# Optimization experiments

Measured on AMD Instinct MI355X. Metric: run time of the kernel, lower is better.

Reference implementation:

```python
import jax, jax.numpy as jnp
import numpy as np

C = 128      # hidden_channels
H = 4        # heads
DH = C // H
G = 4096     # num genes (segments)
R = 4096     # num reactions
E = 65536    # total (reaction, gene) pairs
LMAX = 64    # padded segment length
NB = 4       # blocks: 2 encoder SABs + 1 PMA + 1 decoder SAB
EPS = 1e-5


def _ln(x, g, b):
    m = jnp.mean(x, axis=-1, keepdims=True)
    v = jnp.mean((x - m) ** 2, axis=-1, keepdims=True)
    return (x - m) * jax.lax.rsqrt(v + EPS) * g + b


def setup_inputs() -> dict:
    key = jax.random.key(0)
    ks = jax.random.split(key, 12)
    sc = 1.0 / np.sqrt(C)
    zb = jnp.zeros((NB, C), jnp.float32)
    ob = jnp.ones((NB, C), jnp.float32)
    # every gene gets >= 1 reaction (matches realistic GEM mapping; avoids empty segments)
    gene_idx = jnp.sort(jnp.concatenate([
        jnp.arange(G, dtype=jnp.int32),
        jax.random.randint(ks[8], (E - G,), 0, G, jnp.int32)]))
    return {
        'reaction_features': jax.random.normal(ks[0], (R, C), jnp.float32),
        'Wq': jax.random.normal(ks[1], (NB, C, C), jnp.float32) * sc,
        'Wk': jax.random.normal(ks[2], (NB, C, C), jnp.float32) * sc,
        'Wv': jax.random.normal(ks[3], (NB, C, C), jnp.float32) * sc,
        'Wo': jax.random.normal(ks[4], (NB, C, C), jnp.float32) * sc,
        'bq': zb, 'bk': zb, 'bv': zb, 'bo': zb,
        'Wlin': jax.random.normal(ks[5], (NB, C, C), jnp.float32) * sc,
        'blin': zb,
        'g1': ob, 'b1': zb, 'g2': ob, 'b2': zb,
        'seed': jax.random.normal(ks[6], (1, 1, C), jnp.float32) * sc,
        'rxn_idx': jax.random.randint(ks[7], (E,), 0, R, jnp.int32),
        'gene_idx': gene_idx,
        'num_genes': G,
        'Lmax': LMAX,
    }


def _forward(reaction_features, Wq, Wk, Wv, Wo, bq, bk, bv, bo, Wlin, blin,
             g1, b1, g2, b2, seed, rxn_idx, gene_idx, num_genes, Lmax):
    E_ = gene_idx.shape[0]
    feats = reaction_features[rxn_idx]                      # [E, C] gather
    counts = jax.ops.segment_sum(jnp.ones((E_,), jnp.int32), gene_idx,
                                 num_segments=num_genes)
    starts = jnp.cumsum(counts) - counts                    # first flat index of each segment
    pos = jnp.arange(E_, dtype=jnp.int32) - starts[gene_idx]
    # to_dense_batch: [G, Lmax, C] + mask
    x = jnp.zeros((num_genes, Lmax, C), feats.dtype).at[gene_idx, pos].set(feats, mode='drop')
    mask = jnp.zeros((num_genes, Lmax), bool).at[gene_idx, pos].set(True, mode='drop')

    def mab(q_in, kv_in, q_mask, kv_mask, i):
        B, Lq, _ = q_in.shape
        Lk = kv_in.shape[1]
        q = (q_in @ Wq[i] + bq[i]).reshape(B, Lq, H, DH)
        k = (kv_in @ Wk[i] + bk[i]).reshape(B, Lk, H, DH)
        v = (kv_in @ Wv[i] + bv[i]).reshape(B, Lk, H, DH)
        scores = jnp.einsum('bqhd,bkhd->bhqk', q, k) / np.sqrt(DH)
        if kv_mask is not None:
            scores = jnp.where(kv_mask[:, None, None, :], scores, -1e30)
        a = jax.nn.softmax(scores, axis=-1)
        attn = jnp.einsum('bhqk,bkhd->bqhd', a, v).reshape(B, Lq, C) @ Wo[i] + bo[i]
        if q_mask is not None:
            attn = jnp.where(q_mask[:, :, None], attn, 0.0)
        out = _ln(attn + q_in, g1[i], b1[i])
        out = out + jax.nn.relu(out @ Wlin[i] + blin[i])
        return _ln(out, g2[i], b2[i])

    h = mab(x, x, mask, mask, 0)          # encoder SAB 1
    h = mab(h, h, mask, mask, 1)          # encoder SAB 2
    s = jnp.broadcast_to(seed, (num_genes, seed.shape[1], C))
    h = mab(s, h, None, mask, 2)          # PMA (1 seed point)
    h = mab(h, h, None, None, 3)          # decoder SAB
    h = jnp.nan_to_num(h)
    return h.reshape(num_genes, -1)       # [G, C] (concat over 1 seed)


def reference(reaction_features, Wq, Wk, Wv, Wo, bq, bk, bv, bo, Wlin, blin,
              g1, b1, g2, b2, seed, rxn_idx, gene_idx, num_genes, Lmax):
    return _forward(reaction_features, Wq, Wk, Wv, Wo, bq, bk, bv, bo, Wlin,
                    blin, g1, b1, g2, b2, seed, rxn_idx, gene_idx, num_genes, Lmax)
```

## Files before the change

### kernel.cpp

```cpp
#include <hip/hip_runtime.h>
#include <hip/hip_bf16.h>
#include <math.h>

#define C 128
#define H 4
#define LMAX 64
#define EPS 1e-5f
#define ISQ 0.17677669529663687f

using short8  = __attribute__((ext_vector_type(8))) short;
using short4v = __attribute__((ext_vector_type(4))) short;
using f32x4   = __attribute__((ext_vector_type(4))) float;

__device__ __forceinline__ float wsum(float v){
  #pragma unroll
  for (int o = 32; o > 0; o >>= 1) v += __shfl_xor(v, o, 64);
  return v;
}
__device__ __forceinline__ float wmax(float v){
  #pragma unroll
  for (int o = 32; o > 0; o >>= 1) v = fmaxf(v, __shfl_xor(v, o, 64));
  return v;
}
__device__ __forceinline__ short f2bs(float f){
  __hip_bfloat16 b = __float2bfloat16(f);
  union { __hip_bfloat16 b; short u; } cv; cv.b = b; return cv.u;
}
__device__ __forceinline__ float b2f(short u){
  return __uint_as_float(((unsigned)(unsigned short)u) << 16);
}

__global__ void prep_wfrag(const float* __restrict__ Wq, const float* __restrict__ Wk,
                           const float* __restrict__ Wv, const float* __restrict__ Wo,
                           const float* __restrict__ Wlin, short* __restrict__ wf){
  int bid = blockIdx.x, l = threadIdx.x;
  int tile = bid & 31, mb = bid >> 5;
  int mat = mb >> 2, blk = mb & 3;
  const float* W = (mat==0?Wq : mat==1?Wk : mat==2?Wv : mat==3?Wo : Wlin) + blk*C*C;
  int nt = tile >> 2, kt = tile & 3;
  int col = nt*16 + (l & 15);
  int k0  = kt*32 + ((l >> 4) << 3);
  short8 v;
  #pragma unroll
  for (int j = 0; j < 8; j++) v[j] = f2bs(W[(k0 + j)*C + col]);
  *(short8*)(wf + ((size_t)mb*32 + tile)*512 + (size_t)l*8) = v;
}

__global__ void prep_qrow(const float* __restrict__ seed, const float* __restrict__ Wq,
                          const float* __restrict__ bq, float* __restrict__ qrow){
  int t = threadIdx.x;
  const float* wq2 = Wq + 2*C*C;
  float acc = bq[2*C + t];
  #pragma unroll 4
  for (int k = 0; k < C; k++) acc = fmaf(seed[k], wq2[k*C + t], acc);
  qrow[t] = acc;
}

__global__ void seg_kernel(const int* __restrict__ gidx, int E, int G,
                           int* __restrict__ starts, int* __restrict__ counts,
                           int* __restrict__ cnt, int* __restrict__ gcr){
  int g = blockIdx.x * blockDim.x + threadIdx.x;
  if (g >= G) return;
  int lo = 0, hi = E;
  while (lo < hi){ int m = (lo + hi) >> 1; if (gidx[m] < g) lo = m + 1; else hi = m; }
  int s = lo; hi = E;
  while (lo < hi){ int m = (lo + hi) >> 1; if (gidx[m] < g + 1) lo = m + 1; else hi = m; }
  starts[g] = s;
  int c_ = lo - s; counts[g] = c_;
  int L = c_ > LMAX ? LMAX : c_; if (L < 1) L = 1;
  int cl = (L - 1) >> 4;
  int r = atomicAdd(&cnt[cl], 1);
  gcr[g] = (cl << 28) | r;
}

__global__ void fill_kernel(int G, const int* __restrict__ cnt, const int* __restrict__ gcr,
                            int* __restrict__ binfo, int* __restrict__ nbins){
  int g = blockIdx.x * blockDim.x + threadIdx.x;
  if (g >= G) return;
  int nb1 = (cnt[0] + 3) >> 2, nb2 = (cnt[1] + 1) >> 1, nb3 = cnt[2];
  if (g == 0) *nbins = nb1 + nb2 + nb3 + cnt[3];
  int v = gcr[g]; int cl = v >> 28; int r = v & 0x0FFFFFFF;
  int bin, slot;
  if      (cl == 0){ bin = r >> 2;             slot = r & 3; }
  else if (cl == 1){ bin = nb1 + (r >> 1);     slot = (r & 1) * 2; }
  else if (cl == 2){ bin = nb1 + nb2 + r;      slot = 0; }
  else             { bin = nb1 + nb2 + nb3 + r; slot = 0; }
  binfo[bin*4 + slot] = g;
}

__device__ __forceinline__ f32x4 mfma4(short8 a0, short8 a1, short8 a2, short8 a3,
                                       const short* __restrict__ wf, int nt, int l){
  f32x4 acc = {0.f, 0.f, 0.f, 0.f};
  acc = __builtin_amdgcn_mfma_f32_16x16x32_bf16(a0, *(const short8*)(wf + ((nt*4+0)*64 + l)*8), acc, 0,0,0);
  acc = __builtin_amdgcn_mfma_f32_16x16x32_bf16(a1, *(const short8*)(wf + ((nt*4+1)*64 + l)*8), acc, 0,0,0);
  acc = __builtin_amdgcn_mfma_f32_16x16x32_bf16(a2, *(const short8*)(wf + ((nt*4+2)*64 + l)*8), acc, 0,0,0);
  acc = __builtin_amdgcn_mfma_f32_16x16x32_bf16(a3, *(const short8*)(wf + ((nt*4+3)*64 + l)*8), acc, 0,0,0);
  return acc;
}

__device__ __forceinline__ void ln_rows(const short (*src)[136], short (*dst)[136],
                                        const float* __restrict__ gg,
                                        const float* __restrict__ bb, int t){
  int row = t >> 2, q4 = t & 3;
  float v[32];
  float sm = 0.f;
  #pragma unroll
  for (int kk = 0; kk < 32; ++kk){
    float x = b2f(src[row][q4*32 + kk]);
    v[kk] = x; sm += x;
  }
  sm += __shfl_xor(sm, 1);
  sm += __shfl_xor(sm, 2);
  float mean = sm * (1.f/128.f);
  float s2 = 0.f;
  #pragma unroll
  for (int kk = 0; kk < 32; ++kk){ float d = v[kk] - mean; s2 += d*d; }
  s2 += __shfl_xor(s2, 1);
  s2 += __shfl_xor(s2, 2);
  float rs = rsqrtf(s2*(1.f/128.f) + EPS);
  #pragma unroll
  for (int kk = 0; kk < 32; ++kk){
    int col = q4*32 + kk;
    dst[row][col] = f2bs((v[kk] - mean)*rs*gg[col] + bb[col]);
  }
}

__global__ __launch_bounds__(256, 2) void gene_bin_kernel(
  const float* __restrict__ RF, const short* __restrict__ wfrag,
  const float* __restrict__ qrow,
  const float* __restrict__ bq, const float* __restrict__ bk,
  const float* __restrict__ bv, const float* __restrict__ bo,
  const float* __restrict__ blin,
  const float* __restrict__ g1, const float* __restrict__ b1,
  const float* __restrict__ g2, const float* __restrict__ b2,
  const int* __restrict__ rxn_idx, const int* __restrict__ starts,
  const int* __restrict__ counts, const int* __restrict__ binfo,
  const int* __restrict__ meta, float* __restrict__ pooled)
{
  if ((int)blockIdx.x >= meta[0]) return;
  __shared__ short xb[64][136];
  __shared__ short qb[64][136];
  __shared__ short kb[64][136];
  __shared__ short vt[128][72];
  __shared__ __align__(16) short sc[64][72];
  __shared__ float qrl[C];
  __shared__ int mg[4], mL[4], ms0[4], mbase[4];

  const int bin = blockIdx.x;
  const int t = threadIdx.x, w = t >> 6, l = t & 63;
  const int hi = l >> 4, c = l & 15;

  if (t == 0){
    int s = 0;
    while (s < 4){
      int g = binfo[bin*4 + s];
      if (g >= 0){
        int Lg = counts[g]; if (Lg > LMAX) Lg = LMAX;
        int ntg = (Lg + 15) >> 4;
        for (int u = 0; u < ntg; ++u){ mg[s+u] = g; mL[s+u] = Lg; ms0[s+u] = starts[g]; mbase[s+u] = s; }
        s += ntg;
      } else { mg[s] = -1; mL[s] = 0; ms0[s] = 0; mbase[s] = s; s++; }
    }
  }
  if (t < C) qrl[t] = qrow[t];
  __syncthreads();

  for (int idx = t; idx < 64*16; idx += 256){
    int row = idx >> 4, ch = idx & 15;
    int s = row >> 4;
    int g = mg[s];
    int ro = row - mbase[s]*16;
    short8 u = {0,0,0,0,0,0,0,0};
    if (g >= 0 && ro < mL[s]){
      int rr = rxn_idx[ms0[s] + ro];
      const float* src = RF + (size_t)rr*C + ch*8;
      float4 v0 = *(const float4*)(src);
      float4 v1 = *(const float4*)(src + 4);
      u[0]=f2bs(v0.x); u[1]=f2bs(v0.y); u[2]=f2bs(v0.z); u[3]=f2bs(v0.w);
      u[4]=f2bs(v1.x); u[5]=f2bs(v1.y); u[6]=f2bs(v1.z); u[7]=f2bs(v1.w);
    }
    *(short8*)&xb[row][ch*8] = u;
  }
  {
    short8 z = {0,0,0,0,0,0,0,0};
    for (int idx = t; idx < 64*9; idx += 256){
      int row = idx / 9, ch = idx - row*9;
      *(short8*)&sc[row][ch*8] = z;
    }
  }
  __syncthreads();

  for (int blk = 0; blk < 2; ++blk){
    {
      short8 ax[4][4];
      #pragma unroll
      for (int mt = 0; mt < 4; ++mt)
        #pragma unroll
        for (int kk = 0; kk < 4; ++kk)
          ax[mt][kk] = *(const short8*)&xb[mt*16 + c][kk*32 + hi*8];
      #pragma unroll
      for (int i = 0; i < 6; ++i){
        int pr = w + 4*i;
        int mat = pr >> 3, nt = pr & 7;
        const short* wfm = wfrag + (size_t)(mat*4 + blk)*16384;
        const float* bias = (mat == 0 ? bq : mat == 1 ? bk : bv);
        int col = nt*16 + c;
        float bb = bias[blk*C + col];
        #pragma unroll
        for (int mt = 0; mt < 4; ++mt){
          f32x4 acc = mfma4(ax[mt][0], ax[mt][1], ax[mt][2], ax[mt][3], wfm, nt, l);
          if (mat == 2){
            short4v pk;
            #pragma unroll
            for (int r = 0; r < 4; r++) pk[r] = f2bs(acc[r] + bb);
            *(short4v*)&vt[col][mt*16 + hi*4] = pk;
          } else if (mat == 0){
            #pragma unroll
            for (int r = 0; r < 4; r++) qb[mt*16 + hi*4 + r][col] = f2bs(acc[r] + bb);
          } else {
            #pragma unroll
            for (int r = 0; r < 4; r++) kb[mt*16 + hi*4 + r][col] = f2bs(acc[r] + bb);
          }
        }
      }
    }
    __syncthreads();

    for (int h = 0; h < H; ++h){
      for (int idx = w; idx < 16; idx += 4){
        int mt = idx >> 2, kt = idx & 3;
        int gm = mg[mt];
        if (gm >= 0 && gm == mg[kt]){
          short8 a = *(const short8*)&qb[mt*16 + c][h*32 + hi*8];
          short8 b = *(const short8*)&kb[kt*16 + c][h*32 + hi*8];
          f32x4 acc = {0.f, 0.f, 0.f, 0.f};
          acc = __builtin_amdgcn_mfma_f32_16x16x32_bf16(a, b, acc, 0,0,0);
          #pragma unroll
          for (int r = 0; r < 4; r++) sc[mt*16 + hi*4 + r][kt*16 + c] = f2bs(acc[r] * ISQ);
        }
      }
      __syncthreads();
      {
        int row = t >> 2, q4 = t & 3;
        int s = row >> 4;
        if (mg[s] >= 0){
          int kbeg = mbase[s]*16;
          int kend = kbeg + mL[s];
          int send = kbeg + (((mL[s] + 15) >> 4) << 4);
          int b0 = q4*16;
          float e[16];
          float mx = -3.4e38f;
          #pragma unroll
          for (int kk = 0; kk < 16; ++kk){
            int col = b0 + kk;
            bool ok = (col >= kbeg) && (col < kend);
            float lg = ok ? b2f(sc[row][col]) : -3.4e38f;
            e[kk] = lg;
            mx = fmaxf(mx, lg);
          }
          mx = fmaxf(mx, __shfl_xor(mx, 1));
          mx = fmaxf(mx, __shfl_xor(mx, 2));
          float sm = 0.f;
          #pragma unroll
          for (int kk = 0; kk < 16; ++kk){
            int col = b0 + kk;
            bool ok = (col >= kbeg) && (col < kend);
            float ee = ok ? __expf(e[kk] - mx) : 0.f;
            e[kk] = ee; sm += ee;
          }
          sm += __shfl_xor(sm, 1);
          sm += __shfl_xor(sm, 2);
          float inv = 1.f / sm;
          #pragma unroll
          for (int kk = 0; kk < 16; ++kk){
            int col = b0 + kk;
            if (col >= kbeg && col < send)
              sc[row][col] = f2bs((col < kend) ? e[kk]*inv : 0.f);
          }
        }
      }
      __syncthreads();
      for (int idx = w; idx < 8; idx += 4){
        int mt = idx >> 1, dt = idx & 1;
        if (mg[mt] >= 0){
          f32x4 acc = {0.f, 0.f, 0.f, 0.f};
          #pragma unroll
          for (int ks = 0; ks < 2; ++ks){
            short8 a = *(const short8*)&sc[mt*16 + c][ks*32 + hi*8];
            short8 b = *(const short8*)&vt[h*32 + dt*16 + c][ks*32 + hi*8];
            acc = __builtin_amdgcn_mfma_f32_16x16x32_bf16(a, b, acc, 0,0,0);
          }
          int col = h*32 + dt*16 + c;
          #pragma unroll
          for (int r = 0; r < 4; r++) qb[mt*16 + hi*4 + r][col] = f2bs(acc[r]);
        }
      }
      __syncthreads();
    }

    {
      short8 aw[4];
      #pragma unroll
      for (int kk = 0; kk < 4; kk++) aw[kk] = *(const short8*)&qb[w*16 + c][kk*32 + hi*8];
      const short* wfo = wfrag + (size_t)(3*4 + blk)*16384;
      #pragma unroll 2
      for (int nt = 0; nt < 8; ++nt){
        int col = nt*16 + c;
        f32x4 acc = mfma4(aw[0], aw[1], aw[2], aw[3], wfo, nt, l);
        float bb = bo[blk*C + col];
        #pragma unroll
        for (int r = 0; r < 4; r++){
          int row = w*16 + hi*4 + r;
          xb[row][col] = f2bs(acc[r] + bb + b2f(xb[row][col]));
        }
      }
    }
    __syncthreads();
    ln_rows(xb, xb, g1 + blk*C, b1 + blk*C, t);
    __syncthreads();

    {
      short8 aw[4];
      #pragma unroll
      for (int kk = 0; kk < 4; kk++) aw[kk] = *(const short8*)&xb[w*16 + c][kk*32 + hi*8];
      const short* wfl = wfrag + (size_t)(4*4 + blk)*16384;
      #pragma unroll 2
      for (int nt = 0; nt < 8; ++nt){
        int col = nt*16 + c;
        f32x4 acc = mfma4(aw[0], aw[1], aw[2], aw[3], wfl, nt, l);
        float bb = blin[blk*C + col];
        #pragma unroll
        for (int r = 0; r < 4; r++){
          int row = w*16 + hi*4 + r;
          kb[row][col] = f2bs(b2f(xb[row][col]) + fmaxf(acc[r] + bb, 0.f));
        }
      }
    }
    __syncthreads();
    ln_rows(kb, xb, g2 + blk*C, b2 + blk*C, t);
    __syncthreads();
  }

  {
    short8 aw[4];
    #pragma unroll
    for (int kk = 0; kk < 4; kk++) aw[kk] = *(const short8*)&xb[w*16 + c][kk*32 + hi*8];
    const short* wfk2 = wfrag + (size_t)(1*4 + 2)*16384;
    const short* wfv2 = wfrag + (size_t)(2*4 + 2)*16384;
    #pragma unroll 2
    for (int nt = 0; nt < 8; ++nt){
      int col = nt*16 + c;
      f32x4 acc = mfma4(aw[0], aw[1], aw[2], aw[3], wfk2, nt, l);
      float bb = bk[2*C + col];
      #pragma unroll
      for (int r = 0; r < 4; r++) kb[w*16 + hi*4 + r][col] = f2bs(acc[r] + bb);
      acc = mfma4(aw[0], aw[1], aw[2], aw[3], wfv2, nt, l);
      bb = bv[2*C + col];
      short4v pk;
      #pragma unroll
      for (int r = 0; r < 4; r++) pk[r] = f2bs(acc[r] + bb);
      *(short4v*)&vt[col][w*16 + hi*4] = pk;
    }
  }
  __syncthreads();
  {
    int g = mg[w];
    if (g >= 0 && mbase[w] == w){
      int L = mL[w];
      int row = w*16 + l;
      float* ps = (float*)&sc[0][0];
      #pragma unroll
      for (int h = 0; h < 4; ++h){
        float a = -3.4e38f;
        if (l < L){
          float acc = 0.f;
          #pragma unroll 8
          for (int dd = 0; dd < 32; ++dd)
            acc = fmaf(b2f(kb[row][h*32 + dd]), qrl[h*32 + dd], acc);
          a = acc * ISQ;
        }
        float mx = wmax(a);
        float e = (l < L) ? __expf(a - mx) : 0.f;
        float s = wsum(e);
        ps[(w*4 + h)*64 + l] = e / s;
      }
      #pragma unroll
      for (int half = 0; half < 2; ++half){
        int d = l + half*64;
        int h = d >> 5;
        float acc = 0.f;
        for (int kk = 0; kk < L; ++kk)
          acc = fmaf(ps[(w*4 + h)*64 + kk], b2f(vt[d][w*16 + kk]), acc);
        pooled[(size_t)g*C + d] = acc;
      }
    }
  }
}

__global__ __launch_bounds__(256) void tail_kernel(
  const float* __restrict__ pooled,
  const float* __restrict__ Wv, const float* __restrict__ Wo,
  const float* __restrict__ Wlin,
  const float* __restrict__ bv, const float* __restrict__ bo,
  const float* __restrict__ blin,
  const float* __restrict__ g1, const float* __restrict__ b1,
  const float* __restrict__ g2, const float* __restrict__ b2,
  const float* __restrict__ seed, float* __restrict__ out)
{
  __shared__ float row0[C], row1[C], row2[C];
  const int g = blockIdx.x, t = threadIdx.x, w = t >> 6, l = t & 63;
  if (t < C) row1[t] = pooled[(size_t)g*C + t];
  __syncthreads();
  if (t < C){
    float acc = bo[2*C + t];
    const float* wo2 = Wo + 2*C*C;
    #pragma unroll 4
    for (int k = 0; k < C; k++) acc = fmaf(row1[k], wo2[k*C + t], acc);
    row0[t] = acc + seed[t];
  }
  __syncthreads();
  if (w == 0){
    float v0 = row0[l], v1 = row0[l + 64];
    float m = wsum(v0 + v1) * (1.f / C);
    float d0 = v0 - m, d1 = v1 - m;
    float va = wsum(d0*d0 + d1*d1) * (1.f / C);
    float rs = rsqrtf(va + EPS);
    row0[l]      = d0 * rs * g1[2*C + l]      + b1[2*C + l];
    row0[l + 64] = d1 * rs * g1[2*C + l + 64] + b1[2*C + l + 64];
  }
  __syncthreads();
  if (t < C){
    float acc = blin[2*C + t];
    const float* wl2 = Wlin + 2*C*C;
    #pragma unroll 4
    for (int k = 0; k < C; k++) acc = fmaf(row0[k], wl2[k*C + t], acc);
    row1[t] = row0[t] + fmaxf(acc, 0.f);
  }
  __syncthreads();
  if (w == 0){
    float v0 = row1[l], v1 = row1[l + 64];
    float m = wsum(v0 + v1) * (1.f / C);
    float d0 = v0 - m, d1 = v1 - m;
    float va = wsum(d0*d0 + d1*d1) * (1.f / C);
    float rs = rsqrtf(va + EPS);
    row0[l]      = d0 * rs * g2[2*C + l]      + b2[2*C + l];
    row0[l + 64] = d1 * rs * g2[2*C + l + 64] + b2[2*C + l + 64];
  }
  __syncthreads();
  {
    const float* wv3 = Wv + 3*C*C; const float* wo3 = Wo + 3*C*C; const float* wl3 = Wlin + 3*C*C;
    if (t < C){
      float acc = bv[3*C + t];
      #pragma unroll 4
      for (int k = 0; k < C; k++) acc = fmaf(row0[k], wv3[k*C + t], acc);
      row1[t] = acc;
    }
    __syncthreads();
    if (t < C){
      float acc = bo[3*C + t];
      #pragma unroll 4
      for (int k = 0; k < C; k++) acc = fmaf(row1[k], wo3[k*C + t], acc);
      row2[t] = acc + row0[t];
    }
    __syncthreads();
    if (w == 0){
      float v0 = row2[l], v1 = row2[l + 64];
      float m = wsum(v0 + v1) * (1.f / C);
      float d0 = v0 - m, d1 = v1 - m;
      float va = wsum(d0*d0 + d1*d1) * (1.f / C);
      float rs = rsqrtf(va + EPS);
      row2[l]      = d0 * rs * g1[3*C + l]      + b1[3*C + l];
      row2[l + 64] = d1 * rs * g1[3*C + l + 64] + b1[3*C + l + 64];
    }
    __syncthreads();
    if (t < C){
      float acc = blin[3*C + t];
      #pragma unroll 4
      for (int k = 0; k < C; k++) acc = fmaf(row2[k], wl3[k*C + t], acc);
      row1[t] = row2[t] + fmaxf(acc, 0.f);
    }
    __syncthreads();
    if (w == 0){
      float v0 = row1[l], v1 = row1[l + 64];
      float m = wsum(v0 + v1) * (1.f / C);
      float d0 = v0 - m, d1 = v1 - m;
      float va = wsum(d0*d0 + d1*d1) * (1.f / C);
      float rs = rsqrtf(va + EPS);
      float r0 = d0 * rs * g2[3*C + l]      + b2[3*C + l];
      float r1 = d1 * rs * g2[3*C + l + 64] + b2[3*C + l + 64];
      if (isnan(r0)) r0 = 0.f; else if (isinf(r0)) r0 = r0 > 0 ? 3.402823466e38f : -3.402823466e38f;
      if (isnan(r1)) r1 = 0.f; else if (isinf(r1)) r1 = r1 > 0 ? 3.402823466e38f : -3.402823466e38f;
      out[(size_t)g*C + l]      = r0;
      out[(size_t)g*C + l + 64] = r1;
    }
  }
}

extern "C" void kernel_launch(void* const* d_in, const int* in_sizes, int n_in,
                              void* d_out, int out_size, void* d_ws, size_t ws_size,
                              hipStream_t stream){
  const float* RF   = (const float*)d_in[0];
  const float* Wq   = (const float*)d_in[1];
  const float* Wk   = (const float*)d_in[2];
  const float* Wv   = (const float*)d_in[3];
  const float* Wo   = (const float*)d_in[4];
  const float* bq   = (const float*)d_in[5];
  const float* bk   = (const float*)d_in[6];
  const float* bv   = (const float*)d_in[7];
  const float* bo   = (const float*)d_in[8];
  const float* Wlin = (const float*)d_in[9];
  const float* blin = (const float*)d_in[10];
  const float* g1   = (const float*)d_in[11];
  const float* b1   = (const float*)d_in[12];
  const float* g2   = (const float*)d_in[13];
  const float* b2   = (const float*)d_in[14];
  const float* seed = (const float*)d_in[15];
  const int* rxn    = (const int*)d_in[16];
  const int* gidx   = (const int*)d_in[17];

  int E = in_sizes[16];
  int G = out_size / C;

  char* base = (char*)d_ws;
  short* wfrag = (short*)base;
  float* qrow  = (float*)(base + 655360);
  int*   meta  = (int*)(base + 655872);
  int*   starts= (int*)(base + 655936);
  int*   counts= (int*)(base + 655936 + (size_t)4*G);
  int*   gcr   = (int*)(base + 655936 + (size_t)8*G);
  int*   binfo = (int*)(base + 655936 + (size_t)12*G);
  float* pooled= (float*)(base + 655936 + (size_t)28*G);

  hipMemsetAsync(meta, 0, 64, stream);
  hipMemsetAsync(binfo, 0xFF, (size_t)16*G, stream);
  prep_wfrag<<<640, 64, 0, stream>>>(Wq, Wk, Wv, Wo, Wlin, wfrag);
  prep_qrow<<<1, 128, 0, stream>>>(seed, Wq, bq, qrow);
  seg_kernel<<<(G + 255)/256, 256, 0, stream>>>(gidx, E, G, starts, counts, meta + 1, gcr);
  fill_kernel<<<(G + 255)/256, 256, 0, stream>>>(G, meta + 1, gcr, binfo, meta);
  gene_bin_kernel<<<G, 256, 0, stream>>>(RF, wfrag, qrow, bq, bk, bv, bo, blin,
      g1, b1, g2, b2, rxn, starts, counts, binfo, meta, pooled);
  tail_kernel<<<G, 256, 0, stream>>>(pooled, Wv, Wo, Wlin, bv, bo, blin,
      g1, b1, g2, b2, seed, (float*)d_out);
}
```

Measured before the change: 310.1 us.

## Restructure gene-bin kernel per-wave with in-register softmax/LN and batch tail kernel

The gene-bin kernel now gives each wave its own 16-row tile. Q/K/V projection, attention scores, softmax, layernorm and the residual all stay in registers, which removes the score scratch buffer and most block-wide barriers. Shared memory shrinks (qb, sc and qrl are dropped, rows are padded to 138) and occupancy is raised to 3 blocks per SM. PV MFMAs are skipped for key tiles outside the segment. The tail kernel now handles 16 genes per block, so weight reads are amortised across rows, at the cost of higher register pressure and more intricate per-wave LDS reuse.

```diff
diff --git a/kernel.cpp b/kernel.cpp
--- a/kernel.cpp
+++ b/kernel.cpp
@@ -3,14 +3,14 @@
 #include <math.h>
 
 #define C 128
-#define H 4
 #define LMAX 64
 #define EPS 1e-5f
 #define ISQ 0.17677669529663687f
 
 using short8  = __attribute__((ext_vector_type(8))) short;
-using short4v = __attribute__((ext_vector_type(4))) short;
 using f32x4   = __attribute__((ext_vector_type(4))) float;
+
+#define WSYNC() do { asm volatile("s_waitcnt lgkmcnt(0)" ::: "memory"); __builtin_amdgcn_sched_barrier(0); } while(0)
 
 __device__ __forceinline__ float wsum(float v){
   #pragma unroll
@@ -28,6 +28,9 @@
 }
 __device__ __forceinline__ float b2f(short u){
   return __uint_as_float(((unsigned)(unsigned short)u) << 16);
+}
+__device__ __forceinline__ unsigned pack2(float a, float b){
+  return (unsigned)(unsigned short)f2bs(a) | ((unsigned)(unsigned short)f2bs(b) << 16);
 }
 
 __global__ void prep_wfrag(const float* __restrict__ Wq, const float* __restrict__ Wk,
@@ -98,34 +101,25 @@
   return acc;
 }
 
-__device__ __forceinline__ void ln_rows(const short (*src)[136], short (*dst)[136],
-                                        const float* __restrict__ gg,
-                                        const float* __restrict__ bb, int t){
-  int row = t >> 2, q4 = t & 3;
-  float v[32];
-  float sm = 0.f;
-  #pragma unroll
-  for (int kk = 0; kk < 32; ++kk){
-    float x = b2f(src[row][q4*32 + kk]);
-    v[kk] = x; sm += x;
-  }
-  sm += __shfl_xor(sm, 1);
-  sm += __shfl_xor(sm, 2);
-  float mean = sm * (1.f/128.f);
-  float s2 = 0.f;
-  #pragma unroll
-  for (int kk = 0; kk < 32; ++kk){ float d = v[kk] - mean; s2 += d*d; }
-  s2 += __shfl_xor(s2, 1);
-  s2 += __shfl_xor(s2, 2);
-  float rs = rsqrtf(s2*(1.f/128.f) + EPS);
-  #pragma unroll
-  for (int kk = 0; kk < 32; ++kk){
-    int col = q4*32 + kk;
-    dst[row][col] = f2bs((v[kk] - mean)*rs*gg[col] + bb[col]);
-  }
-}
-
-__global__ __launch_bounds__(256, 2) void gene_bin_kernel(
+__device__ __forceinline__ void ln_inreg(float (&v)[8][4], const float (&gv)[8], const float (&bv)[8]){
+  #pragma unroll
+  for (int r = 0; r < 4; ++r){
+    float s = 0.f;
+    #pragma unroll
+    for (int nt = 0; nt < 8; ++nt) s += v[nt][r];
+    s += __shfl_xor(s,1); s += __shfl_xor(s,2); s += __shfl_xor(s,4); s += __shfl_xor(s,8);
+    float mean = s * (1.f/128.f);
+    float q = 0.f;
+    #pragma unroll
+    for (int nt = 0; nt < 8; ++nt){ float d = v[nt][r] - mean; q += d*d; }
+    q += __shfl_xor(q,1); q += __shfl_xor(q,2); q += __shfl_xor(q,4); q += __shfl_xor(q,8);
+    float rs = rsqrtf(q*(1.f/128.f) + EPS);
+    #pragma unroll
+    for (int nt = 0; nt < 8; ++nt) v[nt][r] = (v[nt][r] - mean)*rs*gv[nt] + bv[nt];
+  }
+}
+
+__global__ __launch_bounds__(256, 3) void gene_bin_kernel(
   const float* __restrict__ RF, const short* __restrict__ wfrag,
   const float* __restrict__ qrow,
   const float* __restrict__ bq, const float* __restrict__ bk,
@@ -137,18 +131,16 @@
   const int* __restrict__ counts, const int* __restrict__ binfo,
   const int* __restrict__ meta, float* __restrict__ pooled)
 {
+  __shared__ short xb[64][138];
+  __shared__ short kb[64][138];
+  __shared__ short vt[128][74];
+  __shared__ int mg[4], mL[4], ms0[4], mbase[4];
+
   if ((int)blockIdx.x >= meta[0]) return;
-  __shared__ short xb[64][136];
-  __shared__ short qb[64][136];
-  __shared__ short kb[64][136];
-  __shared__ short vt[128][72];
-  __shared__ __align__(16) short sc[64][72];
-  __shared__ float qrl[C];
-  __shared__ int mg[4], mL[4], ms0[4], mbase[4];
-
   const int bin = blockIdx.x;
   const int t = threadIdx.x, w = t >> 6, l = t & 63;
   const int hi = l >> 4, c = l & 15;
+  const int r0 = w * 16;
 
   if (t == 0){
     int s = 0;
@@ -162,7 +154,6 @@
       } else { mg[s] = -1; mL[s] = 0; ms0[s] = 0; mbase[s] = s; s++; }
     }
   }
-  if (t < C) qrl[t] = qrow[t];
   __syncthreads();
 
   for (int idx = t; idx < 64*16; idx += 256){
@@ -181,220 +172,271 @@
     }
     *(short8*)&xb[row][ch*8] = u;
   }
-  {
-    short8 z = {0,0,0,0,0,0,0,0};
-    for (int idx = t; idx < 64*9; idx += 256){
-      int row = idx / 9, ch = idx - row*9;
-      *(short8*)&sc[row][ch*8] = z;
-    }
-  }
-  __syncthreads();
-
+  __syncthreads();
+
+  const int myg  = mg[w];
+  const int kbeg = mbase[w]*16;
+  const int kend = kbeg + mL[w];
+
+  float resid[8][4];
+  #pragma unroll
+  for (int nt = 0; nt < 8; ++nt)
+    #pragma unroll
+    for (int r = 0; r < 4; ++r)
+      resid[nt][r] = b2f(xb[r0 + hi*4 + r][nt*16 + c]);
+  WSYNC();
+
+  #pragma unroll 1
   for (int blk = 0; blk < 2; ++blk){
+    const short* wfq = wfrag + (size_t)(0*4 + blk)*16384;
+    const short* wfk = wfrag + (size_t)(1*4 + blk)*16384;
+    const short* wfv = wfrag + (size_t)(2*4 + blk)*16384;
+    const short* wfo = wfrag + (size_t)(3*4 + blk)*16384;
+    const short* wfl = wfrag + (size_t)(4*4 + blk)*16384;
+
     {
-      short8 ax[4][4];
-      #pragma unroll
-      for (int mt = 0; mt < 4; ++mt)
+      short8 ax[4];
+      #pragma unroll
+      for (int kk = 0; kk < 4; ++kk) ax[kk] = *(const short8*)&xb[r0 + c][kk*32 + hi*8];
+      WSYNC();
+      #pragma unroll
+      for (int nt = 0; nt < 8; ++nt){
+        int col = nt*16 + c;
+        f32x4 aq = mfma4(ax[0],ax[1],ax[2],ax[3], wfq, nt, l);
+        f32x4 ak = mfma4(ax[0],ax[1],ax[2],ax[3], wfk, nt, l);
+        f32x4 av = mfma4(ax[0],ax[1],ax[2],ax[3], wfv, nt, l);
+        float bqv = bq[blk*C + col], bkv = bk[blk*C + col], bvv = bv[blk*C + col];
         #pragma unroll
-        for (int kk = 0; kk < 4; ++kk)
-          ax[mt][kk] = *(const short8*)&xb[mt*16 + c][kk*32 + hi*8];
-      #pragma unroll
-      for (int i = 0; i < 6; ++i){
-        int pr = w + 4*i;
-        int mat = pr >> 3, nt = pr & 7;
-        const short* wfm = wfrag + (size_t)(mat*4 + blk)*16384;
-        const float* bias = (mat == 0 ? bq : mat == 1 ? bk : bv);
-        int col = nt*16 + c;
-        float bb = bias[blk*C + col];
+        for (int r = 0; r < 4; ++r){
+          kb[r0 + hi*4 + r][col] = f2bs(ak[r] + bkv);
+          vt[col][r0 + hi*4 + r] = f2bs(av[r] + bvv);
+          xb[r0 + hi*4 + r][col] = f2bs(aq[r] + bqv);
+        }
+      }
+    }
+    __syncthreads();
+
+    unsigned pp[4][8];
+    #pragma unroll
+    for (int h = 0; h < 4; ++h){
+      short8 qa = *(const short8*)&xb[r0 + c][h*32 + hi*8];
+      f32x4 lg[4];
+      #pragma unroll
+      for (int kt = 0; kt < 4; ++kt){
+        f32x4 z = {0.f,0.f,0.f,0.f};
+        if (myg >= 0 && mg[kt] == myg)
+          z = __builtin_amdgcn_mfma_f32_16x16x32_bf16(qa,
+                *(const short8*)&kb[kt*16 + c][h*32 + hi*8], z, 0,0,0);
+        lg[kt] = z;
+      }
+      float P[4][4];
+      #pragma unroll
+      for (int r = 0; r < 4; ++r){
+        float mx = -3.4e38f;
         #pragma unroll
-        for (int mt = 0; mt < 4; ++mt){
-          f32x4 acc = mfma4(ax[mt][0], ax[mt][1], ax[mt][2], ax[mt][3], wfm, nt, l);
-          if (mat == 2){
-            short4v pk;
-            #pragma unroll
-            for (int r = 0; r < 4; r++) pk[r] = f2bs(acc[r] + bb);
-            *(short4v*)&vt[col][mt*16 + hi*4] = pk;
-          } else if (mat == 0){
-            #pragma unroll
-            for (int r = 0; r < 4; r++) qb[mt*16 + hi*4 + r][col] = f2bs(acc[r] + bb);
-          } else {
-            #pragma unroll
-            for (int r = 0; r < 4; r++) kb[mt*16 + hi*4 + r][col] = f2bs(acc[r] + bb);
+        for (int kt = 0; kt < 4; ++kt){
+          int col = kt*16 + c;
+          bool ok = (col >= kbeg) && (col < kend);
+          float v = ok ? lg[kt][r]*ISQ : -3.4e38f;
+          P[kt][r] = v;
+          mx = fmaxf(mx, v);
+        }
+        mx = fmaxf(mx, __shfl_xor(mx,1)); mx = fmaxf(mx, __shfl_xor(mx,2));
+        mx = fmaxf(mx, __shfl_xor(mx,4)); mx = fmaxf(mx, __shfl_xor(mx,8));
+        float sm = 0.f;
+        #pragma unroll
+        for (int kt = 0; kt < 4; ++kt){
+          int col = kt*16 + c;
+          bool ok = (col >= kbeg) && (col < kend);
+          float e = ok ? __expf(P[kt][r] - mx) : 0.f;
+          P[kt][r] = e; sm += e;
+        }
+        sm += __shfl_xor(sm,1); sm += __shfl_xor(sm,2);
+        sm += __shfl_xor(sm,4); sm += __shfl_xor(sm,8);
+        float inv = (sm > 0.f) ? 1.f/sm : 0.f;
+        #pragma unroll
+        for (int kt = 0; kt < 4; ++kt) P[kt][r] *= inv;
+      }
+      #pragma unroll
+      for (int kt = 0; kt < 4; ++kt){
+        pp[h][kt*2+0] = pack2(P[kt][0], P[kt][1]);
+        pp[h][kt*2+1] = pack2(P[kt][2], P[kt][3]);
+      }
+    }
+    __syncthreads();
+
+    f32x4 O[8];
+    {
+      f32x4 zz = {0.f,0.f,0.f,0.f};
+      #pragma unroll
+      for (int nt = 0; nt < 8; ++nt) O[nt] = zz;
+    }
+    #pragma unroll
+    for (int pr = 0; pr < 2; ++pr){
+      #pragma unroll
+      for (int hh = 0; hh < 2; ++hh){
+        int h = pr*2 + hh;
+        #pragma unroll
+        for (int kt = 0; kt < 4; ++kt)
+          #pragma unroll
+          for (int r = 0; r < 4; ++r){
+            unsigned u = pp[h][kt*2 + (r>>1)];
+            xb[r0 + hi*4 + r][hh*64 + kt*16 + c] = (short)((r&1) ? (u >> 16) : (u & 0xFFFF));
           }
-        }
-      }
-    }
-    __syncthreads();
-
-    for (int h = 0; h < H; ++h){
-      for (int idx = w; idx < 16; idx += 4){
-        int mt = idx >> 2, kt = idx & 3;
-        int gm = mg[mt];
-        if (gm >= 0 && gm == mg[kt]){
-          short8 a = *(const short8*)&qb[mt*16 + c][h*32 + hi*8];
-          short8 b = *(const short8*)&kb[kt*16 + c][h*32 + hi*8];
-          f32x4 acc = {0.f, 0.f, 0.f, 0.f};
-          acc = __builtin_amdgcn_mfma_f32_16x16x32_bf16(a, b, acc, 0,0,0);
-          #pragma unroll
-          for (int r = 0; r < 4; r++) sc[mt*16 + hi*4 + r][kt*16 + c] = f2bs(acc[r] * ISQ);
-        }
-      }
-      __syncthreads();
-      {
-        int row = t >> 2, q4 = t & 3;
-        int s = row >> 4;
-        if (mg[s] >= 0){
-          int kbeg = mbase[s]*16;
-          int kend = kbeg + mL[s];
-          int send = kbeg + (((mL[s] + 15) >> 4) << 4);
-          int b0 = q4*16;
-          float e[16];
-          float mx = -3.4e38f;
-          #pragma unroll
-          for (int kk = 0; kk < 16; ++kk){
-            int col = b0 + kk;
-            bool ok = (col >= kbeg) && (col < kend);
-            float lg = ok ? b2f(sc[row][col]) : -3.4e38f;
-            e[kk] = lg;
-            mx = fmaxf(mx, lg);
-          }
-          mx = fmaxf(mx, __shfl_xor(mx, 1));
-          mx = fmaxf(mx, __shfl_xor(mx, 2));
-          float sm = 0.f;
-          #pragma unroll
-          for (int kk = 0; kk < 16; ++kk){
-            int col = b0 + kk;
-            bool ok = (col >= kbeg) && (col < kend);
-            float ee = ok ? __expf(e[kk] - mx) : 0.f;
-            e[kk] = ee; sm += ee;
-          }
-          sm += __shfl_xor(sm, 1);
-          sm += __shfl_xor(sm, 2);
-          float inv = 1.f / sm;
-          #pragma unroll
-          for (int kk = 0; kk < 16; ++kk){
-            int col = b0 + kk;
-            if (col >= kbeg && col < send)
-              sc[row][col] = f2bs((col < kend) ? e[kk]*inv : 0.f);
-          }
-        }
-      }
-      __syncthreads();
-      for (int idx = w; idx < 8; idx += 4){
-        int mt = idx >> 1, dt = idx & 1;
-        if (mg[mt] >= 0){
-          f32x4 acc = {0.f, 0.f, 0.f, 0.f};
+      }
+      WSYNC();
+      #pragma unroll
+      for (int hh = 0; hh < 2; ++hh){
+        int h = pr*2 + hh;
+        #pragma unroll
+        for (int dt = 0; dt < 2; ++dt){
+          f32x4 acc = O[h*2 + dt];
           #pragma unroll
           for (int ks = 0; ks < 2; ++ks){
-            short8 a = *(const short8*)&sc[mt*16 + c][ks*32 + hi*8];
-            short8 b = *(const short8*)&vt[h*32 + dt*16 + c][ks*32 + hi*8];
-            acc = __builtin_amdgcn_mfma_f32_16x16x32_bf16(a, b, acc, 0,0,0);
+            if (kend > ks*32 && kbeg < ks*32 + 32){
+              short8 a = *(const short8*)&xb[r0 + c][hh*64 + ks*32 + hi*8];
+              short8 b = *(const short8*)&vt[h*32 + dt*16 + c][ks*32 + hi*8];
+              acc = __builtin_amdgcn_mfma_f32_16x16x32_bf16(a, b, acc, 0,0,0);
+            }
           }
-          int col = h*32 + dt*16 + c;
-          #pragma unroll
-          for (int r = 0; r < 4; r++) qb[mt*16 + hi*4 + r][col] = f2bs(acc[r]);
+          O[h*2 + dt] = acc;
         }
       }
-      __syncthreads();
-    }
-
-    {
-      short8 aw[4];
-      #pragma unroll
-      for (int kk = 0; kk < 4; kk++) aw[kk] = *(const short8*)&qb[w*16 + c][kk*32 + hi*8];
-      const short* wfo = wfrag + (size_t)(3*4 + blk)*16384;
-      #pragma unroll 2
-      for (int nt = 0; nt < 8; ++nt){
-        int col = nt*16 + c;
-        f32x4 acc = mfma4(aw[0], aw[1], aw[2], aw[3], wfo, nt, l);
-        float bb = bo[blk*C + col];
-        #pragma unroll
-        for (int r = 0; r < 4; r++){
-          int row = w*16 + hi*4 + r;
-          xb[row][col] = f2bs(acc[r] + bb + b2f(xb[row][col]));
-        }
-      }
-    }
+      WSYNC();
+    }
+
+    #pragma unroll
+    for (int nt = 0; nt < 8; ++nt)
+      #pragma unroll
+      for (int r = 0; r < 4; ++r)
+        kb[r0 + hi*4 + r][nt*16 + c] = f2bs(O[nt][r]);
+    WSYNC();
+    short8 af[4];
+    #pragma unroll
+    for (int kk = 0; kk < 4; ++kk) af[kk] = *(const short8*)&kb[r0 + c][kk*32 + hi*8];
+    float y[8][4];
+    float g1v[8], b1v[8], g2v[8], b2v[8];
+    #pragma unroll
+    for (int nt = 0; nt < 8; ++nt){
+      int col = nt*16 + c;
+      g1v[nt] = g1[blk*C + col]; b1v[nt] = b1[blk*C + col];
+      g2v[nt] = g2[blk*C + col]; b2v[nt] = b2[blk*C + col];
+      f32x4 acc = mfma4(af[0],af[1],af[2],af[3], wfo, nt, l);
+      float bb = bo[blk*C + col];
+      #pragma unroll
+      for (int r = 0; r < 4; ++r) y[nt][r] = acc[r] + bb + resid[nt][r];
+    }
+    ln_inreg(y, g1v, b1v);
+    #pragma unroll
+    for (int nt = 0; nt < 8; ++nt)
+      #pragma unroll
+      for (int r = 0; r < 4; ++r)
+        kb[r0 + hi*4 + r][nt*16 + c] = f2bs(y[nt][r]);
+    WSYNC();
+    short8 af2[4];
+    #pragma unroll
+    for (int kk = 0; kk < 4; ++kk) af2[kk] = *(const short8*)&kb[r0 + c][kk*32 + hi*8];
+    float ff[8][4];
+    #pragma unroll
+    for (int nt = 0; nt < 8; ++nt){
+      int col = nt*16 + c;
+      f32x4 acc = mfma4(af2[0],af2[1],af2[2],af2[3], wfl, nt, l);
+      float bb = blin[blk*C + col];
+      #pragma unroll
+      for (int r = 0; r < 4; ++r) ff[nt][r] = y[nt][r] + fmaxf(acc[r] + bb, 0.f);
+    }
+    ln_inreg(ff, g2v, b2v);
+    #pragma unroll
+    for (int nt = 0; nt < 8; ++nt)
+      #pragma unroll
+      for (int r = 0; r < 4; ++r){
+        xb[r0 + hi*4 + r][nt*16 + c] = f2bs(ff[nt][r]);
+        resid[nt][r] = ff[nt][r];
+      }
     __syncthreads();
-    ln_rows(xb, xb, g1 + blk*C, b1 + blk*C, t);
-    __syncthreads();
-
-    {
-      short8 aw[4];
-      #pragma unroll
-      for (int kk = 0; kk < 4; kk++) aw[kk] = *(const short8*)&xb[w*16 + c][kk*32 + hi*8];
-      const short* wfl = wfrag + (size_t)(4*4 + blk)*16384;
-      #pragma unroll 2
-      for (int nt = 0; nt < 8; ++nt){
-        int col = nt*16 + c;
-        f32x4 acc = mfma4(aw[0], aw[1], aw[2], aw[3], wfl, nt, l);
-        float bb = blin[blk*C + col];
-        #pragma unroll
-        for (int r = 0; r < 4; r++){
-          int row = w*16 + hi*4 + r;
-          kb[row][col] = f2bs(b2f(xb[row][col]) + fmaxf(acc[r] + bb, 0.f));
-        }
-      }
-    }
-    __syncthreads();
-    ln_rows(kb, xb, g2 + blk*C, b2 + blk*C, t);
-    __syncthreads();
-  }
-
-  {
-    short8 aw[4];
-    #pragma unroll
-    for (int kk = 0; kk < 4; kk++) aw[kk] = *(const short8*)&xb[w*16 + c][kk*32 + hi*8];
+  }
+
+  {
     const short* wfk2 = wfrag + (size_t)(1*4 + 2)*16384;
     const short* wfv2 = wfrag + (size_t)(2*4 + 2)*16384;
-    #pragma unroll 2
+    short8 ax[4];
+    #pragma unroll
+    for (int kk = 0; kk < 4; ++kk) ax[kk] = *(const short8*)&xb[r0 + c][kk*32 + hi*8];
+    #pragma unroll
     for (int nt = 0; nt < 8; ++nt){
       int col = nt*16 + c;
-      f32x4 acc = mfma4(aw[0], aw[1], aw[2], aw[3], wfk2, nt, l);
-      float bb = bk[2*C + col];
-      #pragma unroll
-      for (int r = 0; r < 4; r++) kb[w*16 + hi*4 + r][col] = f2bs(acc[r] + bb);
-      acc = mfma4(aw[0], aw[1], aw[2], aw[3], wfv2, nt, l);
-      bb = bv[2*C + col];
-      short4v pk;
-      #pragma unroll
-      for (int r = 0; r < 4; r++) pk[r] = f2bs(acc[r] + bb);
-      *(short4v*)&vt[col][w*16 + hi*4] = pk;
-    }
-  }
-  __syncthreads();
-  {
-    int g = mg[w];
-    if (g >= 0 && mbase[w] == w){
-      int L = mL[w];
-      int row = w*16 + l;
-      float* ps = (float*)&sc[0][0];
-      #pragma unroll
-      for (int h = 0; h < 4; ++h){
-        float a = -3.4e38f;
-        if (l < L){
-          float acc = 0.f;
-          #pragma unroll 8
-          for (int dd = 0; dd < 32; ++dd)
-            acc = fmaf(b2f(kb[row][h*32 + dd]), qrl[h*32 + dd], acc);
-          a = acc * ISQ;
-        }
-        float mx = wmax(a);
-        float e = (l < L) ? __expf(a - mx) : 0.f;
-        float s = wsum(e);
-        ps[(w*4 + h)*64 + l] = e / s;
-      }
-      #pragma unroll
-      for (int half = 0; half < 2; ++half){
-        int d = l + half*64;
-        int h = d >> 5;
+      f32x4 ak = mfma4(ax[0],ax[1],ax[2],ax[3], wfk2, nt, l);
+      f32x4 av = mfma4(ax[0],ax[1],ax[2],ax[3], wfv2, nt, l);
+      float bkv = bk[2*C + col], bvv = bv[2*C + col];
+      #pragma unroll
+      for (int r = 0; r < 4; ++r){
+        kb[r0 + hi*4 + r][col] = f2bs(ak[r] + bkv);
+        vt[col][r0 + hi*4 + r] = f2bs(av[r] + bvv);
+      }
+    }
+  }
+  __syncthreads();
+
+  if (myg >= 0 && mbase[w] == w){
+    int L = mL[w];
+    float* ps = (float*)&xb[0][0];
+    #pragma unroll
+    for (int h = 0; h < 4; ++h){
+      float a = -3.4e38f;
+      if (l < L){
         float acc = 0.f;
-        for (int kk = 0; kk < L; ++kk)
-          acc = fmaf(ps[(w*4 + h)*64 + kk], b2f(vt[d][w*16 + kk]), acc);
-        pooled[(size_t)g*C + d] = acc;
-      }
-    }
-  }
+        #pragma unroll 8
+        for (int dd = 0; dd < 32; ++dd)
+          acc = fmaf(b2f(kb[r0 + l][h*32 + dd]), qrow[h*32 + dd], acc);
+        a = acc * ISQ;
+      }
+      float mx = wmax(a);
+      float e = (l < L) ? __expf(a - mx) : 0.f;
+      float s = wsum(e);
+      float inv = (s > 0.f) ? 1.f/s : 0.f;
+      ps[(w*4 + h)*64 + l] = e * inv;
+    }
+    WSYNC();
+    #pragma unroll
+    for (int half = 0; half < 2; ++half){
+      int d = l + half*64;
+      int h = d >> 5;
+      float acc = 0.f;
+      for (int kk = 0; kk < L; ++kk)
+        acc = fmaf(ps[(w*4 + h)*64 + kk], b2f(vt[d][r0 + kk]), acc);
+      pooled[(size_t)myg*C + d] = acc;
+    }
+  }
+}
+
+__device__ __forceinline__ void gemmf(const float (*src)[132], const float* __restrict__ W,
+                                      float (&o)[8], int col, int rg){
+  #pragma unroll
+  for (int r = 0; r < 8; ++r) o[r] = 0.f;
+  #pragma unroll 4
+  for (int k = 0; k < 128; ++k){
+    float wv = W[k*C + col];
+    #pragma unroll
+    for (int r = 0; r < 8; ++r) o[r] = fmaf(src[rg*8 + r][k], wv, o[r]);
+  }
+}
+
+__device__ __forceinline__ void ln16f(float (*buf)[132], const float* __restrict__ gg,
+                                      const float* __restrict__ bb, int t){
+  int row = t >> 4, cg = t & 15;
+  float v[8]; float s = 0.f;
+  #pragma unroll
+  for (int k = 0; k < 8; ++k){ v[k] = buf[row][cg*8 + k]; s += v[k]; }
+  s += __shfl_xor(s,1); s += __shfl_xor(s,2); s += __shfl_xor(s,4); s += __shfl_xor(s,8);
+  float mean = s * (1.f/128.f);
+  float q = 0.f;
+  #pragma unroll
+  for (int k = 0; k < 8; ++k){ float d = v[k] - mean; q += d*d; }
+  q += __shfl_xor(q,1); q += __shfl_xor(q,2); q += __shfl_xor(q,4); q += __shfl_xor(q,8);
+  float rs = rsqrtf(q*(1.f/128.f) + EPS);
+  #pragma unroll
+  for (int k = 0; k < 8; ++k)
+    buf[row][cg*8 + k] = (v[k] - mean)*rs*gg[cg*8 + k] + bb[cg*8 + k];
 }
 
 __global__ __launch_bounds__(256) void tail_kernel(
@@ -405,93 +447,80 @@
   const float* __restrict__ blin,
   const float* __restrict__ g1, const float* __restrict__ b1,
   const float* __restrict__ g2, const float* __restrict__ b2,
-  const float* __restrict__ seed, float* __restrict__ out)
+  const float* __restrict__ seed, float* __restrict__ out, int G)
 {
-  __shared__ float row0[C], row1[C], row2[C];
-  const int g = blockIdx.x, t = threadIdx.x, w = t >> 6, l = t & 63;
-  if (t < C) row1[t] = pooled[(size_t)g*C + t];
-  __syncthreads();
-  if (t < C){
-    float acc = bo[2*C + t];
-    const float* wo2 = Wo + 2*C*C;
-    #pragma unroll 4
-    for (int k = 0; k < C; k++) acc = fmaf(row1[k], wo2[k*C + t], acc);
-    row0[t] = acc + seed[t];
-  }
-  __syncthreads();
-  if (w == 0){
-    float v0 = row0[l], v1 = row0[l + 64];
-    float m = wsum(v0 + v1) * (1.f / C);
-    float d0 = v0 - m, d1 = v1 - m;
-    float va = wsum(d0*d0 + d1*d1) * (1.f / C);
-    float rs = rsqrtf(va + EPS);
-    row0[l]      = d0 * rs * g1[2*C + l]      + b1[2*C + l];
-    row0[l + 64] = d1 * rs * g1[2*C + l + 64] + b1[2*C + l + 64];
-  }
-  __syncthreads();
-  if (t < C){
-    float acc = blin[2*C + t];
-    const float* wl2 = Wlin + 2*C*C;
-    #pragma unroll 4
-    for (int k = 0; k < C; k++) acc = fmaf(row0[k], wl2[k*C + t], acc);
-    row1[t] = row0[t] + fmaxf(acc, 0.f);
-  }
-  __syncthreads();
-  if (w == 0){
-    float v0 = row1[l], v1 = row1[l + 64];
-    float m = wsum(v0 + v1) * (1.f / C);
-    float d0 = v0 - m, d1 = v1 - m;
-    float va = wsum(d0*d0 + d1*d1) * (1.f / C);
-    float rs = rsqrtf(va + EPS);
-    row0[l]      = d0 * rs * g2[2*C + l]      + b2[2*C + l];
-    row0[l + 64] = d1 * rs * g2[2*C + l + 64] + b2[2*C + l + 64];
-  }
-  __syncthreads();
-  {
-    const float* wv3 = Wv + 3*C*C; const float* wo3 = Wo + 3*C*C; const float* wl3 = Wlin + 3*C*C;
-    if (t < C){
-      float acc = bv[3*C + t];
-      #pragma unroll 4
-      for (int k = 0; k < C; k++) acc = fmaf(row0[k], wv3[k*C + t], acc);
-      row1[t] = acc;
-    }
-    __syncthreads();
-    if (t < C){
-      float acc = bo[3*C + t];
-      #pragma unroll 4
-      for (int k = 0; k < C; k++) acc = fmaf(row1[k], wo3[k*C + t], acc);
-      row2[t] = acc + row0[t];
-    }
-    __syncthreads();
-    if (w == 0){
-      float v0 = row2[l], v1 = row2[l + 64];
-      float m = wsum(v0 + v1) * (1.f / C);
-      float d0 = v0 - m, d1 = v1 - m;
-      float va = wsum(d0*d0 + d1*d1) * (1.f / C);
-      float rs = rsqrtf(va + EPS);
-      row2[l]      = d0 * rs * g1[3*C + l]      + b1[3*C + l];
-      row2[l + 64] = d1 * rs * g1[3*C + l + 64] + b1[3*C + l + 64];
-    }
-    __syncthreads();
-    if (t < C){
-      float acc = blin[3*C + t];
-      #pragma unroll 4
-      for (int k = 0; k < C; k++) acc = fmaf(row2[k], wl3[k*C + t], acc);
-      row1[t] = row2[t] + fmaxf(acc, 0.f);
-    }
-    __syncthreads();
-    if (w == 0){
-      float v0 = row1[l], v1 = row1[l + 64];
-      float m = wsum(v0 + v1) * (1.f / C);
-      float d0 = v0 - m, d1 = v1 - m;
-      float va = wsum(d0*d0 + d1*d1) * (1.f / C);
-      float rs = rsqrtf(va + EPS);
-      float r0 = d0 * rs * g2[3*C + l]      + b2[3*C + l];
-      float r1 = d1 * rs * g2[3*C + l + 64] + b2[3*C + l + 64];
-      if (isnan(r0)) r0 = 0.f; else if (isinf(r0)) r0 = r0 > 0 ? 3.402823466e38f : -3.402823466e38f;
-      if (isnan(r1)) r1 = 0.f; else if (isinf(r1)) r1 = r1 > 0 ? 3.402823466e38f : -3.402823466e38f;
-      out[(size_t)g*C + l]      = r0;
-      out[(size_t)g*C + l + 64] = r1;
+  __shared__ float ta[16][132];
+  __shared__ float tb[16][132];
+  const int t = threadIdx.x;
+  const int g0 = blockIdx.x * 16;
+  const int col = t & 127, rg = t >> 7;
+  float o[8], res[8];
+
+  {
+    int row = t >> 4, ch = t & 15;
+    float4 v0 = {0,0,0,0}, v1 = {0,0,0,0};
+    if (g0 + row < G){
+      const float* src = pooled + (size_t)(g0 + row)*C + ch*8;
+      v0 = *(const float4*)(src);
+      v1 = *(const float4*)(src + 4);
+    }
+    *(float4*)&ta[row][ch*8] = v0;
+    *(float4*)&ta[row][ch*8 + 4] = v1;
+  }
+  __syncthreads();
+
+  gemmf(ta, Wo + 2*C*C, o, col, rg);
+  {
+    float ss = seed[col], bb = bo[2*C + col];
+    #pragma unroll
+    for (int r = 0; r < 8; ++r) tb[rg*8 + r][col] = o[r] + bb + ss;
+  }
+  __syncthreads();
+  ln16f(tb, g1 + 2*C, b1 + 2*C, t);
+  __syncthreads();
+  gemmf(tb, Wlin + 2*C*C, o, col, rg);
+  {
+    float bb = blin[2*C + col];
+    #pragma unroll
+    for (int r = 0; r < 8; ++r) ta[rg*8 + r][col] = tb[rg*8 + r][col] + fmaxf(o[r] + bb, 0.f);
+  }
+  __syncthreads();
+  ln16f(ta, g2 + 2*C, b2 + 2*C, t);
+  __syncthreads();
+  gemmf(ta, Wv + 3*C*C, o, col, rg);
+  {
+    float bb = bv[3*C + col];
+    #pragma unroll
+    for (int r = 0; r < 8; ++r) tb[rg*8 + r][col] = o[r] + bb;
+  }
+  __syncthreads();
+  gemmf(tb, Wo + 3*C*C, o, col, rg);
+  {
+    float bb = bo[3*C + col];
+    #pragma unroll
+    for (int r = 0; r < 8; ++r) res[r] = ta[rg*8 + r][col];
+    #pragma unroll
+    for (int r = 0; r < 8; ++r) ta[rg*8 + r][col] = o[r] + bb + res[r];
+  }
+  __syncthreads();
+  ln16f(ta, g1 + 3*C, b1 + 3*C, t);
+  __syncthreads();
+  gemmf(ta, Wlin + 3*C*C, o, col, rg);
+  {
+    float bb = blin[3*C + col];
+    #pragma unroll
+    for (int r = 0; r < 8; ++r) tb[rg*8 + r][col] = ta[rg*8 + r][col] + fmaxf(o[r] + bb, 0.f);
+  }
+  __syncthreads();
+  ln16f(tb, g2 + 3*C, b2 + 3*C, t);
+  __syncthreads();
+  for (int idx = t; idx < 16*128; idx += 256){
+    int row = idx >> 7, cc = idx & 127;
+    if (g0 + row < G){
+      float v = tb[row][cc];
+      if (isnan(v)) v = 0.f;
+      else if (isinf(v)) v = v > 0 ? 3.402823466e38f : -3.402823466e38f;
+      out[(size_t)(g0 + row)*C + cc] = v;
     }
   }
 }
@@ -539,6 +568,6 @@
   fill_kernel<<<(G + 255)/256, 256, 0, stream>>>(G, meta + 1, gcr, binfo, meta);
   gene_bin_kernel<<<G, 256, 0, stream>>>(RF, wfrag, qrow, bq, bk, bv, bo, blin,
       g1, b1, g2, b2, rxn, starts, counts, binfo, meta, pooled);
-  tail_kernel<<<G, 256, 0, stream>>>(pooled, Wv, Wo, Wlin, bv, bo, blin,
-      g1, b1, g2, b2, seed, (float*)d_out);
-}
+  tail_kernel<<<(G + 15)/16, 256, 0, stream>>>(pooled, Wv, Wo, Wlin, bv, bo, blin,
+      g1, b1, g2, b2, seed, (float*)d_out, G);
+}
```

Measured after the change: 309.2 us. Within noise of the previous version (-0.3%).
